# Optimization experiments

Measured on AMD Instinct MI355X. Metric: run time of the kernel, lower is better.

The kernel has to match this reference:

```python
import jax, jax.numpy as jnp
import numpy as np

B, T, D, H, FF = 4, 2048, 1024, 16, 4096
HD = D // H
EPS = 1e-5


def layernorm(x, g, b):
    m = jnp.mean(x, axis=-1, keepdims=True)
    v = jnp.var(x, axis=-1, keepdims=True)
    return (x - m) * jax.lax.rsqrt(v + EPS) * g + b


def setup_inputs() -> dict:
    key = jax.random.key(0)
    ks = jax.random.split(key, 12)
    s = lambda fan_in: 1.0 / np.sqrt(fan_in)
    x = jax.random.normal(ks[0], (B, T, D), dtype=jnp.float32)
    mask = jnp.tril(jnp.ones((T, T), dtype=jnp.int32))[None, None]  # [1,1,T,T] causal
    return {
        "x": x,
        "mask": mask,
        "ln1_g": jnp.ones((D,), jnp.float32),
        "ln1_b": jnp.zeros((D,), jnp.float32),
        "ln2_g": jnp.ones((D,), jnp.float32),
        "ln2_b": jnp.zeros((D,), jnp.float32),
        "qkv_w": jax.random.normal(ks[1], (D, 3 * D), jnp.float32) * s(D),
        "out_w": jax.random.normal(ks[2], (D, D), jnp.float32) * s(D),
        "out_b": jnp.zeros((D,), jnp.float32),
        "fc1_w": jax.random.normal(ks[3], (D, FF), jnp.float32) * s(D),
        "fc1_b": jnp.zeros((FF,), jnp.float32),
        "fc2_w": jax.random.normal(ks[4], (FF, D), jnp.float32) * s(FF),
        "fc2_b": jnp.zeros((D,), jnp.float32),
    }


def reference(x, mask, ln1_g, ln1_b, ln2_g, ln2_b, qkv_w, out_w, out_b,
              fc1_w, fc1_b, fc2_w, fc2_b):
    # --- attention sublayer (pre-LN) ---
    h = layernorm(x, ln1_g, ln1_b)
    qkv = h @ qkv_w  # [B,T,3D]
    q, k, v = jnp.split(qkv, 3, axis=-1)
    q = q.reshape(B, T, H, HD).transpose(0, 2, 1, 3)  # [B,H,T,hd]
    k = k.reshape(B, T, H, HD).transpose(0, 2, 1, 3)
    v = v.reshape(B, T, H, HD).transpose(0, 2, 1, 3)
    scale = 1.0 / np.sqrt(HD)
    scores = jnp.einsum('bhqd,bhkd->bhqk', q, k) * scale  # [B,H,T,T]
    scores = jnp.where(mask == 0, -jnp.inf, scores)
    attn = jax.nn.softmax(scores, axis=-1)
    o = jnp.einsum('bhqk,bhkd->bhqd', attn, v)
    o = o.transpose(0, 2, 1, 3).reshape(B, T, D)
    x = x + (o @ out_w + out_b)
    # --- MLP sublayer (pre-LN) ---
    h = layernorm(x, ln2_g, ln2_b)
    h = jax.nn.gelu(h @ fc1_w + fc1_b, approximate=False)
    x = x + (h @ fc2_w + fc2_b)
    return x
```

## Files before the change

kernel.cpp:

```cpp
#include <hip/hip_runtime.h>

typedef unsigned short bfraw;
typedef __attribute__((ext_vector_type(8))) short short8;
typedef __attribute__((ext_vector_type(4))) float f32x4;

__device__ __forceinline__ float b2f(bfraw u){ return __uint_as_float(((unsigned int)u)<<16); }
__device__ __forceinline__ bfraw f2b(float f){
  unsigned int u = __float_as_uint(f);
  return (bfraw)((u + 0x7FFFu + ((u>>16)&1u)) >> 16);
}
__device__ __forceinline__ void store_out(float* p, float v){ *p = v; }
__device__ __forceinline__ void store_out(bfraw* p, float v){ *p = f2b(v); }
__device__ __forceinline__ void gload_lds16(const bfraw* g, short* l) {
  __builtin_amdgcn_global_load_lds((const __attribute__((address_space(1))) void*)g,
                                   (__attribute__((address_space(3))) void*)l, 16, 0, 0);
}
__device__ __forceinline__ unsigned int cvt_pk_bf16(float a, float b) {
  unsigned int r;
  asm("v_cvt_pk_bf16_f32 %0, %1, %2" : "=v"(r) : "v"(a), "v"(b));
  return r;
}

__global__ __launch_bounds__(1024) void transpose_f32_bf16(const float* __restrict__ in,
                                                           bfraw* __restrict__ out,
                                                           int R, int C) {
  __shared__ bfraw tile[64][65];
  const int tx = threadIdx.x, ty = threadIdx.y;
  const int c0 = blockIdx.x*64, r0 = blockIdx.y*64;
  #pragma unroll
  for (int u = 0; u < 4; ++u)
    tile[ty + u*16][tx] = f2b(in[(size_t)(r0 + ty + u*16)*C + c0 + tx]);
  __syncthreads();
  #pragma unroll
  for (int u = 0; u < 4; ++u)
    out[(size_t)(c0 + ty + u*16)*R + r0 + tx] = tile[tx][ty + u*16];
}

__global__ __launch_bounds__(256) void ln_kernel(const float* __restrict__ x,
                                                 const float* __restrict__ g,
                                                 const float* __restrict__ b,
                                                 bfraw* __restrict__ out) {
  const int row = blockIdx.x, tid = threadIdx.x;
  const f32x4 v = ((const f32x4*)(x + (size_t)row*1024))[tid];
  float s  = v[0]+v[1]+v[2]+v[3];
  float s2 = v[0]*v[0]+v[1]*v[1]+v[2]*v[2]+v[3]*v[3];
  #pragma unroll
  for (int off = 1; off < 64; off <<= 1) { s += __shfl_xor(s, off); s2 += __shfl_xor(s2, off); }
  __shared__ float red[8];
  const int wv = tid>>6, ln_ = tid&63;
  if (ln_ == 0) { red[wv] = s; red[4+wv] = s2; }
  __syncthreads();
  float a  = red[0]+red[1]+red[2]+red[3];
  float a2 = red[4]+red[5]+red[6]+red[7];
  float mean = a*(1.0f/1024.0f);
  float var  = a2*(1.0f/1024.0f) - mean*mean;
  float inv  = rsqrtf(var + 1e-5f);
  const f32x4 gr = ((const f32x4*)g)[tid];
  const f32x4 br = ((const f32x4*)b)[tid];
  ushort4 o4;
  o4.x = f2b((v[0]-mean)*inv*gr[0] + br[0]);
  o4.y = f2b((v[1]-mean)*inv*gr[1] + br[1]);
  o4.z = f2b((v[2]-mean)*inv*gr[2] + br[2]);
  o4.w = f2b((v[3]-mean)*inv*gr[3] + br[3]);
  ((ushort4*)(out + (size_t)row*1024))[tid] = o4;
}

template<int EPI, typename OutT>
__global__ __launch_bounds__(256) void gemm_bt(const bfraw* __restrict__ A,
                                               const bfraw* __restrict__ Bt,
                                               const float* __restrict__ bias,
                                               const float* __restrict__ resid,
                                               OutT* __restrict__ C,
                                               int M, int N, int K) {
  __shared__ __align__(16) short As[128*32];
  __shared__ __align__(16) short Bs[128*32];
  const int tid = threadIdx.x;
  const int wave = tid>>6, lane = tid&63;
  const int wm = wave>>1, wn = wave&1;
  const int q = lane>>4, r = lane&15;
  const int bm = blockIdx.x, bn = blockIdx.y;

  const int m0 = tid>>2, c0 = tid&3;
  const bfraw* Ag0 = A  + (size_t)(bm*128      + m0)*K + c0*8;
  const bfraw* Ag1 = A  + (size_t)(bm*128 + 64 + m0)*K + c0*8;
  const bfraw* Bg0 = Bt + (size_t)(bn*128      + m0)*K + c0*8;
  const bfraw* Bg1 = Bt + (size_t)(bn*128 + 64 + m0)*K + c0*8;
  short* Al0 = &As[tid*8];
  short* Al1 = &As[(256+tid)*8];
  short* Bl0 = &Bs[tid*8];
  short* Bl1 = &Bs[(256+tid)*8];

  f32x4 acc[4][4];
  #pragma unroll
  for (int mi = 0; mi < 4; ++mi)
    #pragma unroll
    for (int ni = 0; ni < 4; ++ni)
      acc[mi][ni] = (f32x4){0.f, 0.f, 0.f, 0.f};

  for (int k0 = 0; k0 < K; k0 += 32) {
    __syncthreads();
    gload_lds16(Ag0 + k0, Al0);
    gload_lds16(Ag1 + k0, Al1);
    gload_lds16(Bg0 + k0, Bl0);
    gload_lds16(Bg1 + k0, Bl1);
    __syncthreads();
    short8 af[4], bfr[4];
    #pragma unroll
    for (int mi = 0; mi < 4; ++mi)
      af[mi] = *(const short8*)&As[(wm*64 + mi*16 + r)*32 + q*8];
    #pragma unroll
    for (int ni = 0; ni < 4; ++ni)
      bfr[ni] = *(const short8*)&Bs[(wn*64 + ni*16 + r)*32 + q*8];
    #pragma unroll
    for (int mi = 0; mi < 4; ++mi)
      #pragma unroll
      for (int ni = 0; ni < 4; ++ni)
        acc[mi][ni] = __builtin_amdgcn_mfma_f32_16x16x32_bf16(af[mi], bfr[ni], acc[mi][ni], 0, 0, 0);
  }

  #pragma unroll
  for (int mi = 0; mi < 4; ++mi) {
    #pragma unroll
    for (int ni = 0; ni < 4; ++ni) {
      const int gcol = bn*128 + wn*64 + ni*16 + r;
      float bv = 0.f;
      if constexpr (EPI != 0) bv = bias[gcol];
      #pragma unroll
      for (int rg = 0; rg < 4; ++rg) {
        const int grow = bm*128 + wm*64 + mi*16 + q*4 + rg;
        float val = acc[mi][ni][rg];
        if constexpr (EPI != 0) val += bv;
        if constexpr (EPI == 2) val = 0.5f*val*(1.0f + erff(val*0.70710678118654752f));
        if constexpr (EPI == 1) val += resid[(size_t)grow*N + gcol];
        store_out(&C[(size_t)grow*N + gcol], val);
      }
    }
  }
}

__global__ __launch_bounds__(256) void flash_attn(const bfraw* __restrict__ qkv,
                                                  bfraw* __restrict__ o) {
  __shared__ __align__(16) short Ksh[4096];
  __shared__ __align__(16) short Vts[4096];
  __shared__ __align__(16) short Psh[4096];
  const int tid = threadIdx.x;
  const int w = tid >> 6, lane = tid & 63;
  const int r = lane & 15, qd = lane >> 4;
  const int bb = blockIdx.y >> 4, h = blockIdx.y & 15;
  const size_t hb = (size_t)bb * 2048;
  short* Pw = &Psh[w * 1024];
  const int f0 = tid, f1 = tid + 256;
  const int key0 = f0 >> 3, dc0 = (f0 & 7) * 8;
  const int key1 = f1 >> 3, dc1 = (f1 & 7) * 8;

  for (int pass = 0; pass < 2; ++pass) {
    const int qt = pass ? (31 - (int)blockIdx.x) : (int)blockIdx.x;
    const int q0 = qt * 64;
    const int ntile = qt + 1;

    short8 qf[2];
    {
      const bfraw* qrow = qkv + (hb + q0 + w*16 + r) * 3072 + h*64;
      qf[0] = *(const short8*)(qrow + qd*8);
      qf[1] = *(const short8*)(qrow + qd*8 + 32);
    }

    f32x4 oacc[4];
    #pragma unroll
    for (int nt = 0; nt < 4; ++nt) oacc[nt] = (f32x4){0.f,0.f,0.f,0.f};
    float m_i = -3.0e38f;
    float l_i = 0.f;

    short8 kpre[2], vpre[2];
    {
      const bfraw* b0 = qkv + (hb + key0) * 3072 + h*64 + dc0;
      const bfraw* b1 = qkv + (hb + key1) * 3072 + h*64 + dc1;
      kpre[0] = *(const short8*)(b0 + 1024); vpre[0] = *(const short8*)(b0 + 2048);
      kpre[1] = *(const short8*)(b1 + 1024); vpre[1] = *(const short8*)(b1 + 2048);
    }

    for (int t = 0; t < ntile; ++t) {
      __syncthreads();
      #pragma unroll
      for (int pz = 0; pz < 2; ++pz) {
        const int key = pz ? key1 : key0, dc = pz ? dc1 : dc0;
        *(short8*)&Ksh[key*64 + ((((dc>>3) ^ (key>>3)) & 7) << 3)] = kpre[pz];
        const int kg = key >> 3, k7 = key & 7, dg = dc >> 3;
        #pragma unroll
        for (int i2 = 0; i2 < 8; ++i2)
          Vts[(dc + i2)*64 + (((kg ^ dg) & 7) << 3) + k7] = vpre[pz][i2];
      }
      __syncthreads();
      if (t + 1 < ntile) {
        const int j0n = (t + 1) * 64;
        const bfraw* b0 = qkv + (hb + j0n + key0) * 3072 + h*64 + dc0;
        const bfraw* b1 = qkv + (hb + j0n + key1) * 3072 + h*64 + dc1;
        kpre[0] = *(const short8*)(b0 + 1024); vpre[0] = *(const short8*)(b0 + 2048);
        kpre[1] = *(const short8*)(b1 + 1024); vpre[1] = *(const short8*)(b1 + 2048);
      }

      f32x4 s4[4];
      __builtin_amdgcn_s_setprio(1);
      #pragma unroll
      for (int kt = 0; kt < 4; ++kt) {
        f32x4 a = (f32x4){0.f,0.f,0.f,0.f};
        const int key = kt*16 + r, kgk = key >> 3;
        #pragma unroll
        for (int ks = 0; ks < 2; ++ks) {
          short8 kf8 = *(const short8*)&Ksh[key*64 + ((((qd + ks*4) ^ kgk) & 7) << 3)];
          a = __builtin_amdgcn_mfma_f32_16x16x32_bf16(kf8, qf[ks], a, 0, 0, 0);
        }
        s4[kt] = a;
      }
      __builtin_amdgcn_s_setprio(0);

      const bool diag = (t == qt);
      #pragma unroll
      for (int kt = 0; kt < 4; ++kt)
        #pragma unroll
        for (int rg = 0; rg < 4; ++rg) {
          float v = s4[kt][rg] * 0.125f;
          if (diag && (kt*16 + qd*4 + rg > w*16 + r)) v = -3.0e38f;
          s4[kt][rg] = v;
        }

      float mx = s4[0][0];
      #pragma unroll
      for (int kt = 0; kt < 4; ++kt)
        #pragma unroll
        for (int rg = 0; rg < 4; ++rg) mx = fmaxf(mx, s4[kt][rg]);
      mx = fmaxf(mx, __shfl_xor(mx, 16));
      mx = fmaxf(mx, __shfl_xor(mx, 32));
      const float mn = fmaxf(m_i, mx);
      const float alpha = __expf(m_i - mn);
      m_i = mn;
      l_i *= alpha;

      float lsum = 0.f;
      #pragma unroll
      for (int kt = 0; kt < 4; ++kt) {
        const float p0 = __expf(s4[kt][0] - mn);
        const float p1 = __expf(s4[kt][1] - mn);
        const float p2 = __expf(s4[kt][2] - mn);
        const float p3 = __expf(s4[kt][3] - mn);
        lsum += (p0 + p1) + (p2 + p3);
        uint2 pk;
        pk.x = cvt_pk_bf16(p0, p1);
        pk.y = cvt_pk_bf16(p2, p3);
        *(uint2*)((char*)Pw + r*128 + ((((kt*2 + (qd>>1)) ^ (r&7)) & 7) << 4) + ((qd&1)<<3)) = pk;
      }
      lsum += __shfl_xor(lsum, 16);
      lsum += __shfl_xor(lsum, 32);
      l_i += lsum;
      #pragma unroll
      for (int nt = 0; nt < 4; ++nt)
        #pragma unroll
        for (int rg = 0; rg < 4; ++rg) oacc[nt][rg] *= alpha;

      short8 pf[2];
      #pragma unroll
      for (int ks = 0; ks < 2; ++ks)
        pf[ks] = *(const short8*)&Pw[r*64 + ((((qd + ks*4) ^ (r & 7)) & 7) << 3)];
      __builtin_amdgcn_s_setprio(1);
      #pragma unroll
      for (int nt = 0; nt < 4; ++nt) {
        const int d = nt*16 + r, dg = d >> 3;
        #pragma unroll
        for (int ks = 0; ks < 2; ++ks) {
          short8 vf = *(const short8*)&Vts[d*64 + ((((qd + ks*4) ^ dg) & 7) << 3)];
          oacc[nt] = __builtin_amdgcn_mfma_f32_16x16x32_bf16(vf, pf[ks], oacc[nt], 0, 0, 0);
        }
      }
      __builtin_amdgcn_s_setprio(0);
    }

    const float invl = 1.0f / l_i;
    bfraw* orow = o + (hb + q0 + w*16 + r) * 1024 + h*64;
    #pragma unroll
    for (int nt = 0; nt < 4; ++nt) {
      uint2 ov;
      ov.x = cvt_pk_bf16(oacc[nt][0]*invl, oacc[nt][1]*invl);
      ov.y = cvt_pk_bf16(oacc[nt][2]*invl, oacc[nt][3]*invl);
      *(uint2*)(orow + nt*16 + qd*4) = ov;
    }
  }
}

extern "C" void kernel_launch(void* const* d_in, const int* in_sizes, int n_in,
                              void* d_out, int out_size, void* d_ws, size_t ws_size,
                              hipStream_t stream) {
  (void)in_sizes; (void)n_in;
  const float* x    = (const float*)d_in[0];
  const float* ln1g = (const float*)d_in[2];
  const float* ln1b = (const float*)d_in[3];
  const float* ln2g = (const float*)d_in[4];
  const float* ln2b = (const float*)d_in[5];
  const float* qkvw = (const float*)d_in[6];
  const float* outw = (const float*)d_in[7];
  const float* outb = (const float*)d_in[8];
  const float* fc1w = (const float*)d_in[9];
  const float* fc1b = (const float*)d_in[10];
  const float* fc2w = (const float*)d_in[11];
  const float* fc2b = (const float*)d_in[12];
  float* out = (float*)d_out;

  char* ws = (char*)d_ws;
  size_t off = 0;
  auto alloc = [&](size_t bytes) -> void* { void* p = ws + off; off += (bytes + 255) & ~(size_t)255; return p; };
  bfraw* wt_qkv = (bfraw*)alloc(3072ULL*1024*2);
  bfraw* wt_out = (bfraw*)alloc(1024ULL*1024*2);
  bfraw* wt_fc1 = (bfraw*)alloc(4096ULL*1024*2);
  bfraw* wt_fc2 = (bfraw*)alloc(1024ULL*4096*2);
  bfraw* hbuf   = (bfraw*)alloc(8192ULL*1024*2);
  float* x1     = (float*)alloc(8192ULL*1024*4);
  char*  big    = (char*) alloc(8192ULL*3072*2 + 8192ULL*1024*2);
  bfraw* qkv  = (bfraw*)big;
  bfraw* obuf = (bfraw*)(big + 8192ULL*3072*2);
  bfraw* hf   = (bfraw*)big;

  if (off > ws_size) {
    (void)hipMemsetAsync(d_out, 0x7F, (size_t)out_size*4, stream);
    return;
  }

  dim3 tb(64, 16);
  transpose_f32_bf16<<<dim3(48, 16), tb, 0, stream>>>(qkvw, wt_qkv, 1024, 3072);
  transpose_f32_bf16<<<dim3(16, 16), tb, 0, stream>>>(outw, wt_out, 1024, 1024);
  transpose_f32_bf16<<<dim3(64, 16), tb, 0, stream>>>(fc1w, wt_fc1, 1024, 4096);
  transpose_f32_bf16<<<dim3(16, 64), tb, 0, stream>>>(fc2w, wt_fc2, 4096, 1024);

  ln_kernel<<<8192, 256, 0, stream>>>(x, ln1g, ln1b, hbuf);
  gemm_bt<0, bfraw><<<dim3(64, 24), 256, 0, stream>>>(hbuf, wt_qkv, nullptr, nullptr, qkv, 8192, 3072, 1024);
  flash_attn<<<dim3(16, 64), 256, 0, stream>>>(qkv, obuf);
  gemm_bt<1, float><<<dim3(64, 8), 256, 0, stream>>>(obuf, wt_out, outb, x, x1, 8192, 1024, 1024);
  ln_kernel<<<8192, 256, 0, stream>>>(x1, ln2g, ln2b, hbuf);
  gemm_bt<2, bfraw><<<dim3(64, 32), 256, 0, stream>>>(hbuf, wt_fc1, fc1b, nullptr, hf, 8192, 4096, 1024);
  gemm_bt<1, float><<<dim3(64, 8), 256, 0, stream>>>(hf, wt_fc2, fc2b, x1, out, 8192, 1024, 4096);
}
```

Before: 591.4 us.

## Double-buffer K/V shared tiles in flash attention to cut per-tile barriers

Doubles the K and V shared-memory tiles so the next tile is written to LDS while the current one is consumed by the MFMAs. The register prefetch now reaches two tiles ahead, and the two __syncthreads per iteration become one waitcnt plus barrier at the end of each tile. The aim is to hide LDS store and global-load latency and remove a synchronization point, at the cost of more LDS per block, which may lower occupancy. Correctness relies on the single end-of-iteration barrier to order writes to the alternate buffer against reads of it.

New measurement: 602.5 us. About the same (+1.9%).

```diff
diff --git a/kernel.cpp b/kernel.cpp
--- a/kernel.cpp
+++ b/kernel.cpp
@@ -140,8 +140,8 @@
 
 __global__ __launch_bounds__(256) void flash_attn(const bfraw* __restrict__ qkv,
                                                   bfraw* __restrict__ o) {
-  __shared__ __align__(16) short Ksh[4096];
-  __shared__ __align__(16) short Vts[4096];
+  __shared__ __align__(16) short Ksh[2][4096];
+  __shared__ __align__(16) short Vts[2][4096];
   __shared__ __align__(16) short Psh[4096];
   const int tid = threadIdx.x;
   const int w = tid >> 6, lane = tid & 63;
@@ -153,6 +153,8 @@
   const int key0 = f0 >> 3, dc0 = (f0 & 7) * 8;
   const int key1 = f1 >> 3, dc1 = (f1 & 7) * 8;
 
+  short8 kpre[2], vpre[2];
+
   for (int pass = 0; pass < 2; ++pass) {
     const int qt = pass ? (31 - (int)blockIdx.x) : (int)blockIdx.x;
     const int q0 = qt * 64;
@@ -171,34 +173,55 @@
     float m_i = -3.0e38f;
     float l_i = 0.f;
 
-    short8 kpre[2], vpre[2];
     {
       const bfraw* b0 = qkv + (hb + key0) * 3072 + h*64 + dc0;
       const bfraw* b1 = qkv + (hb + key1) * 3072 + h*64 + dc1;
       kpre[0] = *(const short8*)(b0 + 1024); vpre[0] = *(const short8*)(b0 + 2048);
       kpre[1] = *(const short8*)(b1 + 1024); vpre[1] = *(const short8*)(b1 + 2048);
     }
+    __syncthreads();
+    #pragma unroll
+    for (int pz = 0; pz < 2; ++pz) {
+      const int key = pz ? key1 : key0, dc = pz ? dc1 : dc0;
+      *(short8*)&Ksh[0][key*64 + ((((dc>>3) ^ (key>>3)) & 7) << 3)] = kpre[pz];
+      const int kg = key >> 3, k7 = key & 7, dg = dc >> 3;
+      #pragma unroll
+      for (int i2 = 0; i2 < 8; ++i2)
+        Vts[0][(dc + i2)*64 + (((kg ^ dg) & 7) << 3) + k7] = vpre[pz][i2];
+    }
+    if (ntile > 1) {
+      const bfraw* b0 = qkv + (hb + 64 + key0) * 3072 + h*64 + dc0;
+      const bfraw* b1 = qkv + (hb + 64 + key1) * 3072 + h*64 + dc1;
+      kpre[0] = *(const short8*)(b0 + 1024); vpre[0] = *(const short8*)(b0 + 2048);
+      kpre[1] = *(const short8*)(b1 + 1024); vpre[1] = *(const short8*)(b1 + 2048);
+    }
+    asm volatile("s_waitcnt lgkmcnt(0)" ::: "memory");
+    __builtin_amdgcn_s_barrier();
 
     for (int t = 0; t < ntile; ++t) {
-      __syncthreads();
-      #pragma unroll
-      for (int pz = 0; pz < 2; ++pz) {
-        const int key = pz ? key1 : key0, dc = pz ? dc1 : dc0;
-        *(short8*)&Ksh[key*64 + ((((dc>>3) ^ (key>>3)) & 7) << 3)] = kpre[pz];
-        const int kg = key >> 3, k7 = key & 7, dg = dc >> 3;
-        #pragma unroll
-        for (int i2 = 0; i2 < 8; ++i2)
-          Vts[(dc + i2)*64 + (((kg ^ dg) & 7) << 3) + k7] = vpre[pz][i2];
-      }
-      __syncthreads();
+      const int cur = t & 1;
       if (t + 1 < ntile) {
-        const int j0n = (t + 1) * 64;
+        const int nb = cur ^ 1;
+        #pragma unroll
+        for (int pz = 0; pz < 2; ++pz) {
+          const int key = pz ? key1 : key0, dc = pz ? dc1 : dc0;
+          *(short8*)&Ksh[nb][key*64 + ((((dc>>3) ^ (key>>3)) & 7) << 3)] = kpre[pz];
+          const int kg = key >> 3, k7 = key & 7, dg = dc >> 3;
+          #pragma unroll
+          for (int i2 = 0; i2 < 8; ++i2)
+            Vts[nb][(dc + i2)*64 + (((kg ^ dg) & 7) << 3) + k7] = vpre[pz][i2];
+        }
+      }
+      if (t + 2 < ntile) {
+        const int j0n = (t + 2) * 64;
         const bfraw* b0 = qkv + (hb + j0n + key0) * 3072 + h*64 + dc0;
         const bfraw* b1 = qkv + (hb + j0n + key1) * 3072 + h*64 + dc1;
         kpre[0] = *(const short8*)(b0 + 1024); vpre[0] = *(const short8*)(b0 + 2048);
         kpre[1] = *(const short8*)(b1 + 1024); vpre[1] = *(const short8*)(b1 + 2048);
       }
 
+      const short* Kb = &Ksh[cur][0];
+      const short* Vb = &Vts[cur][0];
       f32x4 s4[4];
       __builtin_amdgcn_s_setprio(1);
       #pragma unroll
@@ -207,7 +230,7 @@
         const int key = kt*16 + r, kgk = key >> 3;
         #pragma unroll
         for (int ks = 0; ks < 2; ++ks) {
-          short8 kf8 = *(const short8*)&Ksh[key*64 + ((((qd + ks*4) ^ kgk) & 7) << 3)];
+          short8 kf8 = *(const short8*)&Kb[key*64 + ((((qd + ks*4) ^ kgk) & 7) << 3)];
           a = __builtin_amdgcn_mfma_f32_16x16x32_bf16(kf8, qf[ks], a, 0, 0, 0);
         }
         s4[kt] = a;
@@ -267,11 +290,14 @@
         const int d = nt*16 + r, dg = d >> 3;
         #pragma unroll
         for (int ks = 0; ks < 2; ++ks) {
-          short8 vf = *(const short8*)&Vts[d*64 + ((((qd + ks*4) ^ dg) & 7) << 3)];
+          short8 vf = *(const short8*)&Vb[d*64 + ((((qd + ks*4) ^ dg) & 7) << 3)];
           oacc[nt] = __builtin_amdgcn_mfma_f32_16x16x32_bf16(vf, pf[ks], oacc[nt], 0, 0, 0);
         }
       }
       __builtin_amdgcn_s_setprio(0);
+
+      asm volatile("s_waitcnt lgkmcnt(0)" ::: "memory");
+      __builtin_amdgcn_s_barrier();
     }
 
     const float invl = 1.0f / l_i;
```

## Double-buffer GEMM LDS tiles and split flash-attn into one query tile per block

Applied to the files above, without the earlier changes.

The GEMM mainloop now uses two LDS buffers. It prefetches the tile two steps ahead with global_load_lds and waits with explicit vmcnt and barriers, so global loads overlap MFMA work instead of being serialized by two __syncthreads per step. The flash attention kernel drops its paired two-pass loop, which balanced causal work by giving each block tiles qt and 31-qt. Each block now handles a single query tile, heaviest first, over twice as many blocks. This adds parallelism and relies on the scheduler to balance load, at the cost of doubling LDS use in the GEMM and possibly lowering occupancy.

Result: slower. 640.3 us (+8.3%).

```diff
diff --git a/kernel.cpp b/kernel.cpp
--- a/kernel.cpp
+++ b/kernel.cpp
@@ -72,8 +72,8 @@
                                                const float* __restrict__ resid,
                                                OutT* __restrict__ C,
                                                int M, int N, int K) {
-  __shared__ __align__(16) short As[128*32];
-  __shared__ __align__(16) short Bs[128*32];
+  __shared__ __align__(16) short As[2][128*32];
+  __shared__ __align__(16) short Bs[2][128*32];
   const int tid = threadIdx.x;
   const int wave = tid>>6, lane = tid&63;
   const int wm = wave>>1, wn = wave&1;
@@ -85,10 +85,13 @@
   const bfraw* Ag1 = A  + (size_t)(bm*128 + 64 + m0)*K + c0*8;
   const bfraw* Bg0 = Bt + (size_t)(bn*128      + m0)*K + c0*8;
   const bfraw* Bg1 = Bt + (size_t)(bn*128 + 64 + m0)*K + c0*8;
-  short* Al0 = &As[tid*8];
-  short* Al1 = &As[(256+tid)*8];
-  short* Bl0 = &Bs[tid*8];
-  short* Bl1 = &Bs[(256+tid)*8];
+
+  auto stage = [&](int k0, int b) {
+    gload_lds16(Ag0 + k0, &As[b][tid*8]);
+    gload_lds16(Ag1 + k0, &As[b][(256+tid)*8]);
+    gload_lds16(Bg0 + k0, &Bs[b][tid*8]);
+    gload_lds16(Bg1 + k0, &Bs[b][(256+tid)*8]);
+  };
 
   f32x4 acc[4][4];
   #pragma unroll
@@ -97,25 +100,30 @@
     for (int ni = 0; ni < 4; ++ni)
       acc[mi][ni] = (f32x4){0.f, 0.f, 0.f, 0.f};
 
-  for (int k0 = 0; k0 < K; k0 += 32) {
-    __syncthreads();
-    gload_lds16(Ag0 + k0, Al0);
-    gload_lds16(Ag1 + k0, Al1);
-    gload_lds16(Bg0 + k0, Bl0);
-    gload_lds16(Bg1 + k0, Bl1);
-    __syncthreads();
+  stage(0, 0);
+  stage(32, 1);
+
+  const int nt = K >> 5;
+  for (int t = 0; t < nt; ++t) {
+    const int cur = t & 1;
+    if (t + 1 < nt) asm volatile("s_waitcnt vmcnt(4)" ::: "memory");
+    else            asm volatile("s_waitcnt vmcnt(0)" ::: "memory");
+    __builtin_amdgcn_s_barrier();
     short8 af[4], bfr[4];
     #pragma unroll
     for (int mi = 0; mi < 4; ++mi)
-      af[mi] = *(const short8*)&As[(wm*64 + mi*16 + r)*32 + q*8];
+      af[mi] = *(const short8*)&As[cur][(wm*64 + mi*16 + r)*32 + q*8];
     #pragma unroll
     for (int ni = 0; ni < 4; ++ni)
-      bfr[ni] = *(const short8*)&Bs[(wn*64 + ni*16 + r)*32 + q*8];
+      bfr[ni] = *(const short8*)&Bs[cur][(wn*64 + ni*16 + r)*32 + q*8];
     #pragma unroll
     for (int mi = 0; mi < 4; ++mi)
       #pragma unroll
       for (int ni = 0; ni < 4; ++ni)
         acc[mi][ni] = __builtin_amdgcn_mfma_f32_16x16x32_bf16(af[mi], bfr[ni], acc[mi][ni], 0, 0, 0);
+    asm volatile("s_waitcnt lgkmcnt(0)" ::: "memory");
+    __builtin_amdgcn_s_barrier();
+    if (t + 2 < nt) stage((t + 2) << 5, cur);
   }
 
   #pragma unroll
@@ -153,136 +161,134 @@
   const int key0 = f0 >> 3, dc0 = (f0 & 7) * 8;
   const int key1 = f1 >> 3, dc1 = (f1 & 7) * 8;
 
-  for (int pass = 0; pass < 2; ++pass) {
-    const int qt = pass ? (31 - (int)blockIdx.x) : (int)blockIdx.x;
-    const int q0 = qt * 64;
-    const int ntile = qt + 1;
-
-    short8 qf[2];
-    {
-      const bfraw* qrow = qkv + (hb + q0 + w*16 + r) * 3072 + h*64;
-      qf[0] = *(const short8*)(qrow + qd*8);
-      qf[1] = *(const short8*)(qrow + qd*8 + 32);
-    }
-
-    f32x4 oacc[4];
-    #pragma unroll
-    for (int nt = 0; nt < 4; ++nt) oacc[nt] = (f32x4){0.f,0.f,0.f,0.f};
-    float m_i = -3.0e38f;
-    float l_i = 0.f;
-
-    short8 kpre[2], vpre[2];
-    {
-      const bfraw* b0 = qkv + (hb + key0) * 3072 + h*64 + dc0;
-      const bfraw* b1 = qkv + (hb + key1) * 3072 + h*64 + dc1;
+  const int qt = 31 - (int)blockIdx.x;
+  const int q0 = qt * 64;
+  const int ntile = qt + 1;
+
+  short8 qf[2];
+  {
+    const bfraw* qrow = qkv + (hb + q0 + w*16 + r) * 3072 + h*64;
+    qf[0] = *(const short8*)(qrow + qd*8);
+    qf[1] = *(const short8*)(qrow + qd*8 + 32);
+  }
+
+  f32x4 oacc[4];
+  #pragma unroll
+  for (int nt = 0; nt < 4; ++nt) oacc[nt] = (f32x4){0.f,0.f,0.f,0.f};
+  float m_i = -3.0e38f;
+  float l_i = 0.f;
+
+  short8 kpre[2], vpre[2];
+  {
+    const bfraw* b0 = qkv + (hb + key0) * 3072 + h*64 + dc0;
+    const bfraw* b1 = qkv + (hb + key1) * 3072 + h*64 + dc1;
+    kpre[0] = *(const short8*)(b0 + 1024); vpre[0] = *(const short8*)(b0 + 2048);
+    kpre[1] = *(const short8*)(b1 + 1024); vpre[1] = *(const short8*)(b1 + 2048);
+  }
+
+  for (int t = 0; t < ntile; ++t) {
+    __syncthreads();
+    #pragma unroll
+    for (int pz = 0; pz < 2; ++pz) {
+      const int key = pz ? key1 : key0, dc = pz ? dc1 : dc0;
+      *(short8*)&Ksh[key*64 + ((((dc>>3) ^ (key>>3)) & 7) << 3)] = kpre[pz];
+      const int kg = key >> 3, k7 = key & 7, dg = dc >> 3;
+      #pragma unroll
+      for (int i2 = 0; i2 < 8; ++i2)
+        Vts[(dc + i2)*64 + (((kg ^ dg) & 7) << 3) + k7] = vpre[pz][i2];
+    }
+    __syncthreads();
+    if (t + 1 < ntile) {
+      const int j0n = (t + 1) * 64;
+      const bfraw* b0 = qkv + (hb + j0n + key0) * 3072 + h*64 + dc0;
+      const bfraw* b1 = qkv + (hb + j0n + key1) * 3072 + h*64 + dc1;
       kpre[0] = *(const short8*)(b0 + 1024); vpre[0] = *(const short8*)(b0 + 2048);
       kpre[1] = *(const short8*)(b1 + 1024); vpre[1] = *(const short8*)(b1 + 2048);
     }
 
-    for (int t = 0; t < ntile; ++t) {
-      __syncthreads();
-      #pragma unroll
-      for (int pz = 0; pz < 2; ++pz) {
-        const int key = pz ? key1 : key0, dc = pz ? dc1 : dc0;
-        *(short8*)&Ksh[key*64 + ((((dc>>3) ^ (key>>3)) & 7) << 3)] = kpre[pz];
-        const int kg = key >> 3, k7 = key & 7, dg = dc >> 3;
-        #pragma unroll
-        for (int i2 = 0; i2 < 8; ++i2)
-          Vts[(dc + i2)*64 + (((kg ^ dg) & 7) << 3) + k7] = vpre[pz][i2];
+    f32x4 s4[4];
+    __builtin_amdgcn_s_setprio(1);
+    #pragma unroll
+    for (int kt = 0; kt < 4; ++kt) {
+      f32x4 a = (f32x4){0.f,0.f,0.f,0.f};
+      const int key = kt*16 + r, kgk = key >> 3;
+      #pragma unroll
+      for (int ks = 0; ks < 2; ++ks) {
+        short8 kf8 = *(const short8*)&Ksh[key*64 + ((((qd + ks*4) ^ kgk) & 7) << 3)];
+        a = __builtin_amdgcn_mfma_f32_16x16x32_bf16(kf8, qf[ks], a, 0, 0, 0);
       }
-      __syncthreads();
-      if (t + 1 < ntile) {
-        const int j0n = (t + 1) * 64;
-        const bfraw* b0 = qkv + (hb + j0n + key0) * 3072 + h*64 + dc0;
-        const bfraw* b1 = qkv + (hb + j0n + key1) * 3072 + h*64 + dc1;
-        kpre[0] = *(const short8*)(b0 + 1024); vpre[0] = *(const short8*)(b0 + 2048);
-        kpre[1] = *(const short8*)(b1 + 1024); vpre[1] = *(const short8*)(b1 + 2048);
+      s4[kt] = a;
+    }
+    __builtin_amdgcn_s_setprio(0);
+
+    const bool diag = (t == qt);
+    #pragma unroll
+    for (int kt = 0; kt < 4; ++kt)
+      #pragma unroll
+      for (int rg = 0; rg < 4; ++rg) {
+        float v = s4[kt][rg] * 0.125f;
+        if (diag && (kt*16 + qd*4 + rg > w*16 + r)) v = -3.0e38f;
+        s4[kt][rg] = v;
       }
 
-      f32x4 s4[4];
-      __builtin_amdgcn_s_setprio(1);
-      #pragma unroll
-      for (int kt = 0; kt < 4; ++kt) {
-        f32x4 a = (f32x4){0.f,0.f,0.f,0.f};
-        const int key = kt*16 + r, kgk = key >> 3;
-        #pragma unroll
-        for (int ks = 0; ks < 2; ++ks) {
-          short8 kf8 = *(const short8*)&Ksh[key*64 + ((((qd + ks*4) ^ kgk) & 7) << 3)];
-          a = __builtin_amdgcn_mfma_f32_16x16x32_bf16(kf8, qf[ks], a, 0, 0, 0);
-        }
-        s4[kt] = a;
+    float mx = s4[0][0];
+    #pragma unroll
+    for (int kt = 0; kt < 4; ++kt)
+      #pragma unroll
+      for (int rg = 0; rg < 4; ++rg) mx = fmaxf(mx, s4[kt][rg]);
+    mx = fmaxf(mx, __shfl_xor(mx, 16));
+    mx = fmaxf(mx, __shfl_xor(mx, 32));
+    const float mn = fmaxf(m_i, mx);
+    const float alpha = __expf(m_i - mn);
+    m_i = mn;
+    l_i *= alpha;
+
+    float lsum = 0.f;
+    #pragma unroll
+    for (int kt = 0; kt < 4; ++kt) {
+      const float p0 = __expf(s4[kt][0] - mn);
+      const float p1 = __expf(s4[kt][1] - mn);
+      const float p2 = __expf(s4[kt][2] - mn);
+      const float p3 = __expf(s4[kt][3] - mn);
+      lsum += (p0 + p1) + (p2 + p3);
+      uint2 pk;
+      pk.x = cvt_pk_bf16(p0, p1);
+      pk.y = cvt_pk_bf16(p2, p3);
+      *(uint2*)((char*)Pw + r*128 + ((((kt*2 + (qd>>1)) ^ (r&7)) & 7) << 4) + ((qd&1)<<3)) = pk;
+    }
+    lsum += __shfl_xor(lsum, 16);
+    lsum += __shfl_xor(lsum, 32);
+    l_i += lsum;
+    #pragma unroll
+    for (int nt = 0; nt < 4; ++nt)
+      #pragma unroll
+      for (int rg = 0; rg < 4; ++rg) oacc[nt][rg] *= alpha;
+
+    short8 pf[2];
+    #pragma unroll
+    for (int ks = 0; ks < 2; ++ks)
+      pf[ks] = *(const short8*)&Pw[r*64 + ((((qd + ks*4) ^ (r & 7)) & 7) << 3)];
+    __builtin_amdgcn_s_setprio(1);
+    #pragma unroll
+    for (int nt = 0; nt < 4; ++nt) {
+      const int d = nt*16 + r, dg = d >> 3;
+      #pragma unroll
+      for (int ks = 0; ks < 2; ++ks) {
+        short8 vf = *(const short8*)&Vts[d*64 + ((((qd + ks*4) ^ dg) & 7) << 3)];
+        oacc[nt] = __builtin_amdgcn_mfma_f32_16x16x32_bf16(vf, pf[ks], oacc[nt], 0, 0, 0);
       }
-      __builtin_amdgcn_s_setprio(0);
-
-      const bool diag = (t == qt);
-      #pragma unroll
-      for (int kt = 0; kt < 4; ++kt)
-        #pragma unroll
-        for (int rg = 0; rg < 4; ++rg) {
-          float v = s4[kt][rg] * 0.125f;
-          if (diag && (kt*16 + qd*4 + rg > w*16 + r)) v = -3.0e38f;
-          s4[kt][rg] = v;
-        }
-
-      float mx = s4[0][0];
-      #pragma unroll
-      for (int kt = 0; kt < 4; ++kt)
-        #pragma unroll
-        for (int rg = 0; rg < 4; ++rg) mx = fmaxf(mx, s4[kt][rg]);
-      mx = fmaxf(mx, __shfl_xor(mx, 16));
-      mx = fmaxf(mx, __shfl_xor(mx, 32));
-      const float mn = fmaxf(m_i, mx);
-      const float alpha = __expf(m_i - mn);
-      m_i = mn;
-      l_i *= alpha;
-
-      float lsum = 0.f;
-      #pragma unroll
-      for (int kt = 0; kt < 4; ++kt) {
-        const float p0 = __expf(s4[kt][0] - mn);
-        const float p1 = __expf(s4[kt][1] - mn);
-        const float p2 = __expf(s4[kt][2] - mn);
-        const float p3 = __expf(s4[kt][3] - mn);
-        lsum += (p0 + p1) + (p2 + p3);
-        uint2 pk;
-        pk.x = cvt_pk_bf16(p0, p1);
-        pk.y = cvt_pk_bf16(p2, p3);
-        *(uint2*)((char*)Pw + r*128 + ((((kt*2 + (qd>>1)) ^ (r&7)) & 7) << 4) + ((qd&1)<<3)) = pk;
-      }
-      lsum += __shfl_xor(lsum, 16);
-      lsum += __shfl_xor(lsum, 32);
-      l_i += lsum;
-      #pragma unroll
-      for (int nt = 0; nt < 4; ++nt)
-        #pragma unroll
-        for (int rg = 0; rg < 4; ++rg) oacc[nt][rg] *= alpha;
-
-      short8 pf[2];
-      #pragma unroll
-      for (int ks = 0; ks < 2; ++ks)
-        pf[ks] = *(const short8*)&Pw[r*64 + ((((qd + ks*4) ^ (r & 7)) & 7) << 3)];
-      __builtin_amdgcn_s_setprio(1);
-      #pragma unroll
-      for (int nt = 0; nt < 4; ++nt) {
-        const int d = nt*16 + r, dg = d >> 3;
-        #pragma unroll
-        for (int ks = 0; ks < 2; ++ks) {
-          short8 vf = *(const short8*)&Vts[d*64 + ((((qd + ks*4) ^ dg) & 7) << 3)];
-          oacc[nt] = __builtin_amdgcn_mfma_f32_16x16x32_bf16(vf, pf[ks], oacc[nt], 0, 0, 0);
-        }
-      }
-      __builtin_amdgcn_s_setprio(0);
-    }
-
-    const float invl = 1.0f / l_i;
-    bfraw* orow = o + (hb + q0 + w*16 + r) * 1024 + h*64;
-    #pragma unroll
-    for (int nt = 0; nt < 4; ++nt) {
-      uint2 ov;
-      ov.x = cvt_pk_bf16(oacc[nt][0]*invl, oacc[nt][1]*invl);
-      ov.y = cvt_pk_bf16(oacc[nt][2]*invl, oacc[nt][3]*invl);
-      *(uint2*)(orow + nt*16 + qd*4) = ov;
-    }
+    }
+    __builtin_amdgcn_s_setprio(0);
+  }
+
+  const float invl = 1.0f / l_i;
+  bfraw* orow = o + (hb + q0 + w*16 + r) * 1024 + h*64;
+  #pragma unroll
+  for (int nt = 0; nt < 4; ++nt) {
+    uint2 ov;
+    ov.x = cvt_pk_bf16(oacc[nt][0]*invl, oacc[nt][1]*invl);
+    ov.y = cvt_pk_bf16(oacc[nt][2]*invl, oacc[nt][3]*invl);
+    *(uint2*)(orow + nt*16 + qd*4) = ov;
   }
 }
 
@@ -331,7 +337,7 @@
 
   ln_kernel<<<8192, 256, 0, stream>>>(x, ln1g, ln1b, hbuf);
   gemm_bt<0, bfraw><<<dim3(64, 24), 256, 0, stream>>>(hbuf, wt_qkv, nullptr, nullptr, qkv, 8192, 3072, 1024);
-  flash_attn<<<dim3(16, 64), 256, 0, stream>>>(qkv, obuf);
+  flash_attn<<<dim3(32, 64), 256, 0, stream>>>(qkv, obuf);
   gemm_bt<1, float><<<dim3(64, 8), 256, 0, stream>>>(obuf, wt_out, outb, x, x1, 8192, 1024, 1024);
   ln_kernel<<<8192, 256, 0, stream>>>(x1, ln2g, ln2b, hbuf);
   gemm_bt<2, bfraw><<<dim3(64, 32), 256, 0, stream>>>(hbuf, wt_fc1, fc1b, nullptr, hf, 8192, 4096, 1024);
```
